# Kernel optimization log

Hardware: AMD Instinct MI355X
Metric: run time of the kernel (lower is better)

The kernel has to match this reference:

```python
import jax, jax.numpy as jnp
import numpy as np

N_NODES = 50000
N_EDGES = 800000
IN_FEAT = 100
OUT_FEAT = 100
NUM_RELS = 200
NUM_HEADS = 3
NUM_BASES = 100
SUB_IN = 1   # in_feat // num_bases
SUB_OUT = 1  # out_feat // num_bases


def setup_inputs() -> dict:
    key = jax.random.key(0)
    ks = jax.random.split(key, 10)
    return {
        "h": jax.random.normal(ks[0], (N_NODES, IN_FEAT), jnp.float32),
        "e": jax.random.normal(ks[1], (N_EDGES, IN_FEAT), jnp.float32),
        "norm": jax.random.uniform(ks[2], (N_NODES, 1), jnp.float32),
        "weight": jax.random.normal(ks[3], (NUM_RELS, NUM_BASES * SUB_IN * SUB_OUT), jnp.float32) * 0.1,
        "attn": jax.random.normal(ks[4], (NUM_RELS, NUM_HEADS, OUT_FEAT), jnp.float32) * 0.1,
        "fc_w": jax.random.normal(ks[5], (IN_FEAT, OUT_FEAT * NUM_HEADS), jnp.float32) * 0.1,
        "loop_w": jax.random.normal(ks[6], (IN_FEAT, OUT_FEAT), jnp.float32) * 0.1,
        "rel": jax.random.randint(ks[7], (N_EDGES,), 0, NUM_RELS, jnp.int32),
        "src": jax.random.randint(ks[8], (N_EDGES,), 0, N_NODES, jnp.int32),
        "dst": jax.random.randint(ks[9], (N_EDGES,), 0, N_NODES, jnp.int32),
    }


def reference(h, e, norm, weight, attn, fc_w, loop_w, rel, src, dst):
    E = rel.shape[0]
    # --- relation-indexed block-diagonal message (torch.bmm over blocks) ---
    W_e = weight[rel].reshape(E, NUM_BASES, SUB_IN, SUB_OUT)        # per-edge block weights
    h_src = h[src].reshape(E, NUM_BASES, SUB_IN)                    # gathered src features
    msg = jnp.einsum('ebi,ebio->ebo', h_src, W_e).reshape(E, OUT_FEAT)
    # --- edge-feature attention fuse ---
    a_e = attn[rel]                                                 # (E, H, OUT)
    fc_e = (e @ fc_w).reshape(E, NUM_HEADS, OUT_FEAT)               # fc(edge)
    feat = jax.nn.leaky_relu(a_e * fc_e, 0.2).sum(axis=1)           # (E, OUT)
    msg = msg + feat
    # --- scatter-sum aggregation to dst nodes, then norm + self-loop ---
    agg = jax.ops.segment_sum(msg, dst, num_segments=N_NODES)       # (N, OUT)
    node = agg * norm
    loop_message = h @ loop_w
    return node + loop_message
```

## Files before the change

### kernel.cpp

```cpp
#include <hip/hip_runtime.h>
#include <hip/hip_bf16.h>

#define N_NODES 50000
#define N_EDGES 800000
#define IN_FEAT 100
#define OUT_FEAT 100
#define NUM_RELS 200
#define NUM_HEADS 3

#define KP 128
#define NPH 112
#define NP  336
#define MB  128
#define NT_O 7
#define WPB 12

#define WS_B       0u
#define WS_LW      86016u
#define WS_CNT     114688u
#define WS_OFFS    315392u
#define WS_CURSOR  516096u
#define WS_BSUM    716800u
#define WS_PERM    717056u
#define WS_MSG     3917056u
#define NNODES_PAD 50176

typedef __attribute__((ext_vector_type(8))) short short8;
typedef __attribute__((ext_vector_type(4))) float f32x4;

__device__ __forceinline__ unsigned short f2bf(float f) {
    unsigned u = __builtin_bit_cast(unsigned, f);
    unsigned r = u + 0x7FFFu + ((u >> 16) & 1u);
    return (unsigned short)(r >> 16);
}
__device__ __forceinline__ float bf2f(unsigned hs) {
    return __builtin_bit_cast(float, hs << 16);
}

__global__ __launch_bounds__(256) void build_B(const float* __restrict__ fc_w,
                                               unsigned short* __restrict__ Bws) {
    int idx = blockIdx.x * 256 + threadIdx.x;
    if (idx >= NP * 16) return;
    int n = idx >> 4, g = idx & 15;
    int head = n / NPH, nl = n - head * NPH;
    int kt = g >> 2, g4 = g & 3;
    unsigned p[4];
#pragma unroll
    for (int half = 0; half < 2; ++half) {
#pragma unroll
        for (int jp = 0; jp < 2; ++jp) {
            int k_lo = kt * 32 + half * 16 + g4 * 4 + jp * 2;
            int k_hi = k_lo + 1;
            float vlo = (k_lo < IN_FEAT && nl < OUT_FEAT)
                      ? fc_w[k_lo * (OUT_FEAT * NUM_HEADS) + head * OUT_FEAT + nl] : 0.f;
            float vhi = (k_hi < IN_FEAT && nl < OUT_FEAT)
                      ? fc_w[k_hi * (OUT_FEAT * NUM_HEADS) + head * OUT_FEAT + nl] : 0.f;
            p[half * 2 + jp] = (unsigned)f2bf(vlo) | ((unsigned)f2bf(vhi) << 16);
        }
    }
    unsigned off = (unsigned)(head * (NPH * KP * 2)) +
                   (((unsigned)(nl * (KP * 2) + g * 16)) ^ (((unsigned)(nl & 7)) << 4));
    *reinterpret_cast<int4*>(reinterpret_cast<char*>(Bws) + off) =
        make_int4((int)p[0], (int)p[1], (int)p[2], (int)p[3]);
}

__global__ __launch_bounds__(256) void build_LW(const float* __restrict__ loop_w,
                                                unsigned short* __restrict__ LWws) {
    int idx = blockIdx.x * 256 + threadIdx.x;
    if (idx >= NPH * 16) return;
    int nl = idx >> 4, g = idx & 15;
    int kt = g >> 2, g4 = g & 3;
    unsigned p[4];
#pragma unroll
    for (int half = 0; half < 2; ++half) {
#pragma unroll
        for (int jp = 0; jp < 2; ++jp) {
            int k_lo = kt * 32 + half * 16 + g4 * 4 + jp * 2;
            int k_hi = k_lo + 1;
            float vlo = (k_lo < IN_FEAT && nl < OUT_FEAT) ? loop_w[k_lo * OUT_FEAT + nl] : 0.f;
            float vhi = (k_hi < IN_FEAT && nl < OUT_FEAT) ? loop_w[k_hi * OUT_FEAT + nl] : 0.f;
            p[half * 2 + jp] = (unsigned)f2bf(vlo) | ((unsigned)f2bf(vhi) << 16);
        }
    }
    reinterpret_cast<int4*>(LWws)[idx] = make_int4((int)p[0], (int)p[1], (int)p[2], (int)p[3]);
}

__global__ __launch_bounds__(512, 2) void loop_gemm(const float* __restrict__ h,
                                                    const unsigned short* __restrict__ LWimg,
                                                    float* __restrict__ out) {
    const int tid = threadIdx.x;
    const int wave = tid >> 6, lane = tid & 63;
    const int lrow = lane & 15, lk = lane >> 4;
    const int rbase = blockIdx.x * MB;
    const int grow = rbase + wave * 16 + lrow;
    const bool ok = grow < N_NODES;
    const float* ap = h + (size_t)grow * IN_FEAT;

    short8 afrag[4];
#pragma unroll
    for (int kt = 0; kt < 4; ++kt) {
        int k0 = kt * 32 + lk * 4, k1 = k0 + 16;
        float4 va = (ok && k0 + 4 <= IN_FEAT) ? *reinterpret_cast<const float4*>(ap + k0)
                                              : make_float4(0.f, 0.f, 0.f, 0.f);
        float4 vb = (ok && k1 + 4 <= IN_FEAT) ? *reinterpret_cast<const float4*>(ap + k1)
                                              : make_float4(0.f, 0.f, 0.f, 0.f);
        afrag[kt][0] = (short)f2bf(va.x); afrag[kt][1] = (short)f2bf(va.y);
        afrag[kt][2] = (short)f2bf(va.z); afrag[kt][3] = (short)f2bf(va.w);
        afrag[kt][4] = (short)f2bf(vb.x); afrag[kt][5] = (short)f2bf(vb.y);
        afrag[kt][6] = (short)f2bf(vb.z); afrag[kt][7] = (short)f2bf(vb.w);
    }

#pragma unroll
    for (int nt = 0; nt < NT_O; ++nt) {
        f32x4 acc = (f32x4){0.f, 0.f, 0.f, 0.f};
#pragma unroll
        for (int kt = 0; kt < 4; ++kt) {
            short8 bfrag = *reinterpret_cast<const short8*>(
                LWimg + ((nt * 16 + lrow) * KP + kt * 32 + lk * 8));
            acc = __builtin_amdgcn_mfma_f32_16x16x32_bf16(afrag[kt], bfrag, acc, 0, 0, 0);
        }
        int o = nt * 16 + lrow;
        if (o < OUT_FEAT) {
#pragma unroll
            for (int r = 0; r < 4; ++r) {
                int crow = rbase + wave * 16 + lk * 4 + r;
                if (crow < N_NODES) out[(size_t)crow * OUT_FEAT + o] = acc[r];
            }
        }
    }
}

__global__ __launch_bounds__(512) void hist_kernel(const int* __restrict__ dst,
                                                   int* __restrict__ cnt) {
    int e = blockIdx.x * 512 + threadIdx.x;
    if (e < N_EDGES) atomicAdd(&cnt[dst[e]], 1);
}

__global__ __launch_bounds__(1024) void scan1(const int* __restrict__ cnt,
                                              int* __restrict__ offs,
                                              int* __restrict__ bsum) {
    __shared__ int s[1024];
    int i = blockIdx.x * 1024 + threadIdx.x;
    int v = (i < N_NODES) ? cnt[i] : 0;
    s[threadIdx.x] = v;
    __syncthreads();
    for (int d = 1; d < 1024; d <<= 1) {
        int t = (threadIdx.x >= d) ? s[threadIdx.x - d] : 0;
        __syncthreads();
        s[threadIdx.x] += t;
        __syncthreads();
    }
    offs[i] = s[threadIdx.x] - v;
    if (threadIdx.x == 1023) bsum[blockIdx.x] = s[1023];
}

__global__ __launch_bounds__(64) void scan2(int* __restrict__ bsum) {
    __shared__ int s[64];
    int v = (threadIdx.x < NNODES_PAD / 1024) ? bsum[threadIdx.x] : 0;
    s[threadIdx.x] = v;
    __syncthreads();
    for (int d = 1; d < 64; d <<= 1) {
        int t = (threadIdx.x >= d) ? s[threadIdx.x - d] : 0;
        __syncthreads();
        s[threadIdx.x] += t;
        __syncthreads();
    }
    bsum[threadIdx.x] = s[threadIdx.x] - v;
}

__global__ __launch_bounds__(1024) void scan3(int* __restrict__ offs,
                                              const int* __restrict__ bsum,
                                              int* __restrict__ cursor) {
    int i = blockIdx.x * 1024 + threadIdx.x;
    int v = offs[i] + bsum[blockIdx.x];
    offs[i] = v;
    cursor[i] = v;
}

__global__ __launch_bounds__(512) void scatter_kernel(const int* __restrict__ dst,
                                                      int* __restrict__ cursor,
                                                      int* __restrict__ perm) {
    int e = blockIdx.x * 512 + threadIdx.x;
    if (e < N_EDGES) {
        int p = atomicAdd(&cursor[dst[e]], 1);
        perm[p] = e;
    }
}

template<bool TOWS>
__global__ __launch_bounds__(768)
__attribute__((amdgpu_waves_per_eu(3, 3)))
void feat_kernel(
        const float* __restrict__ efeat, const int* __restrict__ rel,
        const unsigned short* __restrict__ Bimg, const float* __restrict__ attn,
        const float* __restrict__ h, const float* __restrict__ weight,
        const float* __restrict__ norm, const int* __restrict__ src,
        const int* __restrict__ dst, const int* __restrict__ perm,
        float* __restrict__ out, unsigned short* __restrict__ msgws,
        int lo, int ntiles) {

    __shared__ unsigned short Blds[NP * KP];
    __shared__ unsigned short slice[WPB][16 * NPH];

    const int tid = threadIdx.x;
    {
        const int4* sp = reinterpret_cast<const int4*>(Bimg);
        int4* dp = reinterpret_cast<int4*>(Blds);
        for (int i = tid; i < NP * KP / 8; i += 768) dp[i] = sp[i];
    }
    __syncthreads();

    const int wave = tid >> 6, lane = tid & 63;
    const int lrow = lane & 15, lk = lane >> 4;
    const int gstride = gridDim.x * WPB;
    int tile = blockIdx.x * WPB + wave;
    if (tile >= ntiles) return;

    const char* Bc = reinterpret_cast<const char*>(Blds);
    int bkt[4];
#pragma unroll
    for (int kt = 0; kt < 4; ++kt)
        bkt[kt] = lrow * (KP * 2) + ((kt * 64 + lk * 16) ^ ((lrow & 7) << 4));

    float4 pa[8];
    int rl[4], sr[4], dd[4];
    {
        int slot = lo + tile * 16;
        int pe = TOWS ? perm[slot + lrow] : (slot + lrow);
        const float* ap = efeat + (size_t)pe * IN_FEAT;
#pragma unroll
        for (int kt = 0; kt < 4; ++kt) {
            int k0 = kt * 32 + lk * 4, k1 = k0 + 16;
            pa[kt * 2]     = (k0 + 4 <= IN_FEAT) ? *reinterpret_cast<const float4*>(ap + k0)
                                                 : make_float4(0.f, 0.f, 0.f, 0.f);
            pa[kt * 2 + 1] = (k1 + 4 <= IN_FEAT) ? *reinterpret_cast<const float4*>(ap + k1)
                                                 : make_float4(0.f, 0.f, 0.f, 0.f);
        }
#pragma unroll
        for (int r = 0; r < 4; ++r) {
            int pr = TOWS ? perm[slot + lk * 4 + r] : (slot + lk * 4 + r);
            rl[r] = rel[pr]; sr[r] = src[pr]; dd[r] = dst[pr];
        }
    }

    while (true) {
        const int cur = tile;
        short8 afrag[4];
#pragma unroll
        for (int kt = 0; kt < 4; ++kt) {
            float4 va = pa[kt * 2], vb = pa[kt * 2 + 1];
            afrag[kt][0] = (short)f2bf(va.x); afrag[kt][1] = (short)f2bf(va.y);
            afrag[kt][2] = (short)f2bf(va.z); afrag[kt][3] = (short)f2bf(va.w);
            afrag[kt][4] = (short)f2bf(vb.x); afrag[kt][5] = (short)f2bf(vb.y);
            afrag[kt][6] = (short)f2bf(vb.z); afrag[kt][7] = (short)f2bf(vb.w);
        }
        float nm[4]; int aoff[4]; const float* hp[4]; const float* wp[4]; int ddc[4];
#pragma unroll
        for (int r = 0; r < 4; ++r) {
            nm[r]  = norm[dd[r]];
            aoff[r] = rl[r] * (NUM_HEADS * OUT_FEAT);
            hp[r]  = h + (size_t)sr[r] * IN_FEAT;
            wp[r]  = weight + (size_t)rl[r] * OUT_FEAT;
            ddc[r] = dd[r];
        }
        float feat[NT_O][4];
#pragma unroll
        for (int nt = 0; nt < NT_O; ++nt) {
            int o = nt * 16 + lrow;
#pragma unroll
            for (int r = 0; r < 4; ++r)
                feat[nt][r] = (o < OUT_FEAT) ? hp[r][o] * wp[r][o] : 0.f;
        }
        int next = tile + gstride;
        bool more = next < ntiles;
        {
            int pidx = more ? next : cur;
            int slot = lo + pidx * 16;
            int pe = TOWS ? perm[slot + lrow] : (slot + lrow);
            const float* ap = efeat + (size_t)pe * IN_FEAT;
#pragma unroll
            for (int kt = 0; kt < 4; ++kt) {
                int k0 = kt * 32 + lk * 4, k1 = k0 + 16;
                pa[kt * 2]     = (k0 + 4 <= IN_FEAT) ? *reinterpret_cast<const float4*>(ap + k0)
                                                     : make_float4(0.f, 0.f, 0.f, 0.f);
                pa[kt * 2 + 1] = (k1 + 4 <= IN_FEAT) ? *reinterpret_cast<const float4*>(ap + k1)
                                                     : make_float4(0.f, 0.f, 0.f, 0.f);
            }
#pragma unroll
            for (int r = 0; r < 4; ++r) {
                int pr = TOWS ? perm[slot + lk * 4 + r] : (slot + lk * 4 + r);
                rl[r] = rel[pr]; sr[r] = src[pr]; dd[r] = dst[pr];
            }
        }

#pragma unroll 1
        for (int hh = 0; hh < NUM_HEADS; ++hh) {
            const char* Bh = Bc + hh * (NPH * KP * 2);
#pragma unroll
            for (int nt = 0; nt < NT_O; ++nt) {
                f32x4 acc = (f32x4){0.f, 0.f, 0.f, 0.f};
#pragma unroll
                for (int kt = 0; kt < 4; ++kt) {
                    short8 bfrag = *reinterpret_cast<const short8*>(
                        Bh + bkt[kt] + nt * 4096);
                    acc = __builtin_amdgcn_mfma_f32_16x16x32_bf16(afrag[kt], bfrag, acc, 0, 0, 0);
                }
                int o = nt * 16 + lrow;
                if (o < OUT_FEAT) {
                    int oo = hh * OUT_FEAT + o;
#pragma unroll
                    for (int r = 0; r < 4; ++r) {
                        float v = acc[r] * attn[aoff[r] + oo];
                        feat[nt][r] += (v > 0.f) ? v : 0.2f * v;
                    }
                }
            }
        }

        if (TOWS) {
            unsigned short* sl = slice[wave];
#pragma unroll
            for (int nt = 0; nt < NT_O; ++nt) {
                int o = nt * 16 + lrow;
#pragma unroll
                for (int r = 0; r < 4; ++r)
                    sl[(lk * 4 + r) * NPH + o] = f2bf(feat[nt][r] * nm[r]);
            }
            asm volatile("s_waitcnt lgkmcnt(0)" ::: "memory");
            __builtin_amdgcn_sched_barrier(0);
            const int4* sp = reinterpret_cast<const int4*>(sl);
            int4* gp = reinterpret_cast<int4*>(msgws + (size_t)cur * (16 * NPH));
            gp[lane]       = sp[lane];
            gp[lane + 64]  = sp[lane + 64];
            gp[lane + 128] = sp[lane + 128];
            if (lane < 32) gp[lane + 192] = sp[lane + 192];
        } else {
#pragma unroll
            for (int nt = 0; nt < NT_O; ++nt) {
                int o = nt * 16 + lrow;
                if (o < OUT_FEAT) {
#pragma unroll
                    for (int r = 0; r < 4; ++r)
                        atomicAdd(&out[(size_t)ddc[r] * OUT_FEAT + o], feat[nt][r] * nm[r]);
                }
            }
        }

        if (!more) break;
        tile = next;
    }
}

__global__ __launch_bounds__(256) void agg_kernel(
        const unsigned short* __restrict__ msgws, const int* __restrict__ offs,
        const int* __restrict__ cnt, float* __restrict__ out, int lo, int hi) {
    int wv = threadIdx.x >> 6, lane = threadIdx.x & 63;
    int n = blockIdx.x * 4 + wv;
    if (n >= N_NODES) return;
    int s0 = offs[n], deg = cnt[n];
    int start = s0 > lo ? s0 : lo;
    int end = (s0 + deg) < hi ? (s0 + deg) : hi;
    if (start >= end) return;
    if (lane >= OUT_FEAT / 2) return;
    const unsigned* mp = reinterpret_cast<const unsigned*>(msgws);
    float ax = 0.f, ay = 0.f;
    int k = start;
    for (; k + 2 <= end; k += 2) {
        unsigned u0 = mp[(size_t)(k - lo) * (NPH / 2) + lane];
        unsigned u1 = mp[(size_t)(k + 1 - lo) * (NPH / 2) + lane];
        ax += bf2f(u0 & 0xffffu) + bf2f(u1 & 0xffffu);
        ay += bf2f(u0 >> 16) + bf2f(u1 >> 16);
    }
    if (k < end) {
        unsigned u0 = mp[(size_t)(k - lo) * (NPH / 2) + lane];
        ax += bf2f(u0 & 0xffffu);
        ay += bf2f(u0 >> 16);
    }
    float2* op = reinterpret_cast<float2*>(out + (size_t)n * OUT_FEAT) + lane;
    float2 curv = *op;
    curv.x += ax; curv.y += ay;
    *op = curv;
}

extern "C" void kernel_launch(void* const* d_in, const int* in_sizes, int n_in,
                              void* d_out, int out_size, void* d_ws, size_t ws_size,
                              hipStream_t stream) {
    const float* h      = (const float*)d_in[0];
    const float* efeat  = (const float*)d_in[1];
    const float* norm   = (const float*)d_in[2];
    const float* weight = (const float*)d_in[3];
    const float* attn   = (const float*)d_in[4];
    const float* fc_w   = (const float*)d_in[5];
    const float* loop_w = (const float*)d_in[6];
    const int*   rel    = (const int*)d_in[7];
    const int*   src    = (const int*)d_in[8];
    const int*   dst    = (const int*)d_in[9];
    float* out = (float*)d_out;

    char* ws = (char*)d_ws;
    unsigned short* Bimg  = (unsigned short*)(ws + WS_B);
    unsigned short* LWimg = (unsigned short*)(ws + WS_LW);
    int* cnt    = (int*)(ws + WS_CNT);
    int* offs   = (int*)(ws + WS_OFFS);
    int* cursor = (int*)(ws + WS_CURSOR);
    int* bsum   = (int*)(ws + WS_BSUM);
    int* perm   = (int*)(ws + WS_PERM);
    unsigned short* msgws = (unsigned short*)(ws + WS_MSG);

    build_B<<<(NP * 16 + 255) / 256, 256, 0, stream>>>(fc_w, Bimg);
    build_LW<<<(NPH * 16 + 255) / 256, 256, 0, stream>>>(loop_w, LWimg);
    loop_gemm<<<(N_NODES + MB - 1) / MB, 512, 0, stream>>>(h, LWimg, out);

    long long avail = (long long)ws_size - (long long)WS_MSG;
    long long rows = (avail > 0) ? avail / (NPH * 2) : 0;
    rows = (rows / MB) * MB;
    if (rows > N_EDGES) rows = N_EDGES;

    if (rows >= 100000) {
        hipMemsetAsync(cnt, 0, NNODES_PAD * sizeof(int), stream);
        hist_kernel<<<(N_EDGES + 511) / 512, 512, 0, stream>>>(dst, cnt);
        scan1<<<NNODES_PAD / 1024, 1024, 0, stream>>>(cnt, offs, bsum);
        scan2<<<1, 64, 0, stream>>>(bsum);
        scan3<<<NNODES_PAD / 1024, 1024, 0, stream>>>(offs, bsum, cursor);
        scatter_kernel<<<(N_EDGES + 511) / 512, 512, 0, stream>>>(dst, cursor, perm);

        for (long long lo = 0; lo < N_EDGES; lo += rows) {
            long long hi = lo + rows; if (hi > N_EDGES) hi = N_EDGES;
            int ntiles = (int)((hi - lo) / 16);
            int nb = (ntiles + WPB - 1) / WPB; if (nb > 256) nb = 256;
            feat_kernel<true><<<nb, 768, 0, stream>>>(
                efeat, rel, Bimg, attn, h, weight, norm, src, dst, perm,
                out, msgws, (int)lo, ntiles);
            agg_kernel<<<(N_NODES + 3) / 4, 256, 0, stream>>>(
                msgws, offs, cnt, out, (int)lo, (int)hi);
        }
    } else {
        int ntiles = N_EDGES / 16;
        int nb = (ntiles + WPB - 1) / WPB; if (nb > 256) nb = 256;
        feat_kernel<false><<<nb, 768, 0, stream>>>(
            efeat, rel, Bimg, attn, h, weight, norm, src, dst, nullptr,
            out, msgws, 0, ntiles);
    }
}
```

Measured before the change: 493.6 us.

## Read edges in natural order, scatter messages to dst-sorted slots, fuse h*W in aggregation

The feature kernel now streams edge features and rel in their original order and writes each bf16 message row directly to its dst-sorted slot through a new slotmap, replacing the perm-indexed gather of efeat. The h[src]*weight[rel] product and the norm scaling move out of the feature kernel into the aggregation kernel, which gathers them through perm. Message rows shrink to 100 bf16 values and chunking over the workspace is removed in favour of a single pass. Block size and occupancy hints also change (512 threads, 8 waves per block). The trade is scattered 8-byte stores and extra gathers in agg in exchange for coalesced efeat reads.

```diff
diff --git a/kernel.cpp b/kernel.cpp
--- a/kernel.cpp
+++ b/kernel.cpp
@@ -13,7 +13,9 @@
 #define NP  336
 #define MB  128
 #define NT_O 7
-#define WPB 12
+#define WPB 8
+#define SLP 116
+#define MSGW 100
 
 #define WS_B       0u
 #define WS_LW      86016u
@@ -21,8 +23,10 @@
 #define WS_OFFS    315392u
 #define WS_CURSOR  516096u
 #define WS_BSUM    716800u
-#define WS_PERM    717056u
-#define WS_MSG     3917056u
+#define WS_SLOT    717056u
+#define WS_PERM    3917056u
+#define WS_MSG     7117056u
+#define WS_NEEDED  167117056u
 #define NNODES_PAD 50176
 
 typedef __attribute__((ext_vector_type(8))) short short8;
@@ -179,34 +183,34 @@
 
 __global__ __launch_bounds__(512) void scatter_kernel(const int* __restrict__ dst,
                                                       int* __restrict__ cursor,
-                                                      int* __restrict__ perm) {
+                                                      int* __restrict__ perm,
+                                                      int* __restrict__ slotmap) {
     int e = blockIdx.x * 512 + threadIdx.x;
     if (e < N_EDGES) {
         int p = atomicAdd(&cursor[dst[e]], 1);
         perm[p] = e;
+        slotmap[e] = p;
     }
 }
 
 template<bool TOWS>
-__global__ __launch_bounds__(768)
-__attribute__((amdgpu_waves_per_eu(3, 3)))
-void feat_kernel(
+__global__ __launch_bounds__(512, 2) void feat_kernel(
         const float* __restrict__ efeat, const int* __restrict__ rel,
         const unsigned short* __restrict__ Bimg, const float* __restrict__ attn,
         const float* __restrict__ h, const float* __restrict__ weight,
         const float* __restrict__ norm, const int* __restrict__ src,
-        const int* __restrict__ dst, const int* __restrict__ perm,
+        const int* __restrict__ dst, const int* __restrict__ slotmap,
         float* __restrict__ out, unsigned short* __restrict__ msgws,
-        int lo, int ntiles) {
-
-    __shared__ unsigned short Blds[NP * KP];
-    __shared__ unsigned short slice[WPB][16 * NPH];
+        int ntiles) {
+
+    __shared__ __align__(16) unsigned short Blds[NP * KP];
+    __shared__ __align__(16) unsigned short slice[WPB][16 * SLP];
 
     const int tid = threadIdx.x;
     {
         const int4* sp = reinterpret_cast<const int4*>(Bimg);
         int4* dp = reinterpret_cast<int4*>(Blds);
-        for (int i = tid; i < NP * KP / 8; i += 768) dp[i] = sp[i];
+        for (int i = tid; i < NP * KP / 8; i += 512) dp[i] = sp[i];
     }
     __syncthreads();
 
@@ -223,11 +227,9 @@
         bkt[kt] = lrow * (KP * 2) + ((kt * 64 + lk * 16) ^ ((lrow & 7) << 4));
 
     float4 pa[8];
-    int rl[4], sr[4], dd[4];
+    int prl[4];
     {
-        int slot = lo + tile * 16;
-        int pe = TOWS ? perm[slot + lrow] : (slot + lrow);
-        const float* ap = efeat + (size_t)pe * IN_FEAT;
+        const float* ap = efeat + (size_t)(tile * 16 + lrow) * IN_FEAT;
 #pragma unroll
         for (int kt = 0; kt < 4; ++kt) {
             int k0 = kt * 32 + lk * 4, k1 = k0 + 16;
@@ -236,15 +238,14 @@
             pa[kt * 2 + 1] = (k1 + 4 <= IN_FEAT) ? *reinterpret_cast<const float4*>(ap + k1)
                                                  : make_float4(0.f, 0.f, 0.f, 0.f);
         }
-#pragma unroll
-        for (int r = 0; r < 4; ++r) {
-            int pr = TOWS ? perm[slot + lk * 4 + r] : (slot + lk * 4 + r);
-            rl[r] = rel[pr]; sr[r] = src[pr]; dd[r] = dst[pr];
-        }
+        const int* rp = rel + tile * 16 + lk * 4;
+#pragma unroll
+        for (int r = 0; r < 4; ++r) prl[r] = rp[r];
     }
 
     while (true) {
         const int cur = tile;
+        const int tb = cur * 16;
         short8 afrag[4];
 #pragma unroll
         for (int kt = 0; kt < 4; ++kt) {
@@ -254,30 +255,15 @@
             afrag[kt][4] = (short)f2bf(vb.x); afrag[kt][5] = (short)f2bf(vb.y);
             afrag[kt][6] = (short)f2bf(vb.z); afrag[kt][7] = (short)f2bf(vb.w);
         }
-        float nm[4]; int aoff[4]; const float* hp[4]; const float* wp[4]; int ddc[4];
-#pragma unroll
-        for (int r = 0; r < 4; ++r) {
-            nm[r]  = norm[dd[r]];
-            aoff[r] = rl[r] * (NUM_HEADS * OUT_FEAT);
-            hp[r]  = h + (size_t)sr[r] * IN_FEAT;
-            wp[r]  = weight + (size_t)rl[r] * OUT_FEAT;
-            ddc[r] = dd[r];
-        }
-        float feat[NT_O][4];
-#pragma unroll
-        for (int nt = 0; nt < NT_O; ++nt) {
-            int o = nt * 16 + lrow;
-#pragma unroll
-            for (int r = 0; r < 4; ++r)
-                feat[nt][r] = (o < OUT_FEAT) ? hp[r][o] * wp[r][o] : 0.f;
-        }
+        int aoff[4];
+#pragma unroll
+        for (int r = 0; r < 4; ++r) aoff[r] = prl[r] * (NUM_HEADS * OUT_FEAT);
+
         int next = tile + gstride;
         bool more = next < ntiles;
         {
             int pidx = more ? next : cur;
-            int slot = lo + pidx * 16;
-            int pe = TOWS ? perm[slot + lrow] : (slot + lrow);
-            const float* ap = efeat + (size_t)pe * IN_FEAT;
+            const float* ap = efeat + (size_t)(pidx * 16 + lrow) * IN_FEAT;
 #pragma unroll
             for (int kt = 0; kt < 4; ++kt) {
                 int k0 = kt * 32 + lk * 4, k1 = k0 + 16;
@@ -286,12 +272,16 @@
                 pa[kt * 2 + 1] = (k1 + 4 <= IN_FEAT) ? *reinterpret_cast<const float4*>(ap + k1)
                                                      : make_float4(0.f, 0.f, 0.f, 0.f);
             }
-#pragma unroll
-            for (int r = 0; r < 4; ++r) {
-                int pr = TOWS ? perm[slot + lk * 4 + r] : (slot + lk * 4 + r);
-                rl[r] = rel[pr]; sr[r] = src[pr]; dd[r] = dst[pr];
-            }
-        }
+            const int* rp = rel + pidx * 16 + lk * 4;
+#pragma unroll
+            for (int r = 0; r < 4; ++r) prl[r] = rp[r];
+        }
+
+        float feat[NT_O][4];
+#pragma unroll
+        for (int nt = 0; nt < NT_O; ++nt)
+#pragma unroll
+            for (int r = 0; r < 4; ++r) feat[nt][r] = 0.f;
 
 #pragma unroll 1
         for (int hh = 0; hh < NUM_HEADS; ++hh) {
@@ -322,26 +312,44 @@
 #pragma unroll
             for (int nt = 0; nt < NT_O; ++nt) {
                 int o = nt * 16 + lrow;
-#pragma unroll
-                for (int r = 0; r < 4; ++r)
-                    sl[(lk * 4 + r) * NPH + o] = f2bf(feat[nt][r] * nm[r]);
+                if (o < OUT_FEAT) {
+#pragma unroll
+                    for (int r = 0; r < 4; ++r)
+                        sl[(lk * 4 + r) * SLP + o] = f2bf(feat[nt][r]);
+                }
             }
             asm volatile("s_waitcnt lgkmcnt(0)" ::: "memory");
             __builtin_amdgcn_sched_barrier(0);
-            const int4* sp = reinterpret_cast<const int4*>(sl);
-            int4* gp = reinterpret_cast<int4*>(msgws + (size_t)cur * (16 * NPH));
-            gp[lane]       = sp[lane];
-            gp[lane + 64]  = sp[lane + 64];
-            gp[lane + 128] = sp[lane + 128];
-            if (lane < 32) gp[lane + 192] = sp[lane + 192];
+            const int row = lane >> 2, part = lane & 3;
+            const int slot = slotmap[tb + row];
+            const unsigned long long* sq =
+                reinterpret_cast<const unsigned long long*>(slice[wave]);
+            unsigned long long* mq = reinterpret_cast<unsigned long long*>(msgws);
+#pragma unroll
+            for (int j = 0; j < 7; ++j) {
+                int idx = part + 4 * j;
+                if (idx < 25)
+                    mq[(size_t)slot * 25 + idx] = sq[row * (SLP / 4) + idx];
+            }
         } else {
+            int sr_r[4], d_r[4]; float nm_r[4]; int rl_r[4];
+#pragma unroll
+            for (int r = 0; r < 4; ++r) {
+                int ei = tb + lk * 4 + r;
+                sr_r[r] = src[ei]; d_r[r] = dst[ei]; nm_r[r] = norm[d_r[r]];
+                rl_r[r] = aoff[r] / (NUM_HEADS * OUT_FEAT);
+            }
 #pragma unroll
             for (int nt = 0; nt < NT_O; ++nt) {
                 int o = nt * 16 + lrow;
                 if (o < OUT_FEAT) {
 #pragma unroll
-                    for (int r = 0; r < 4; ++r)
-                        atomicAdd(&out[(size_t)ddc[r] * OUT_FEAT + o], feat[nt][r] * nm[r]);
+                    for (int r = 0; r < 4; ++r) {
+                        float mg = h[(size_t)sr_r[r] * IN_FEAT + o] *
+                                   weight[(size_t)rl_r[r] * OUT_FEAT + o];
+                        atomicAdd(&out[(size_t)d_r[r] * OUT_FEAT + o],
+                                  (mg + feat[nt][r]) * nm_r[r]);
+                    }
                 }
             }
         }
@@ -351,34 +359,46 @@
     }
 }
 
-__global__ __launch_bounds__(256) void agg_kernel(
+__global__ __launch_bounds__(256, 2) void agg_kernel(
         const unsigned short* __restrict__ msgws, const int* __restrict__ offs,
-        const int* __restrict__ cnt, float* __restrict__ out, int lo, int hi) {
+        const int* __restrict__ cnt, const int* __restrict__ perm,
+        const int* __restrict__ src, const int* __restrict__ rel,
+        const float* __restrict__ h, const float* __restrict__ weight,
+        const float* __restrict__ norm, float* __restrict__ out) {
     int wv = threadIdx.x >> 6, lane = threadIdx.x & 63;
     int n = blockIdx.x * 4 + wv;
     if (n >= N_NODES) return;
-    int s0 = offs[n], deg = cnt[n];
-    int start = s0 > lo ? s0 : lo;
-    int end = (s0 + deg) < hi ? (s0 + deg) : hi;
-    if (start >= end) return;
-    if (lane >= OUT_FEAT / 2) return;
+    int start = offs[n], deg = cnt[n];
+    if (deg == 0 || lane >= OUT_FEAT / 2) return;
     const unsigned* mp = reinterpret_cast<const unsigned*>(msgws);
     float ax = 0.f, ay = 0.f;
-    int k = start;
+    int k = start, end = start + deg;
     for (; k + 2 <= end; k += 2) {
-        unsigned u0 = mp[(size_t)(k - lo) * (NPH / 2) + lane];
-        unsigned u1 = mp[(size_t)(k + 1 - lo) * (NPH / 2) + lane];
-        ax += bf2f(u0 & 0xffffu) + bf2f(u1 & 0xffffu);
-        ay += bf2f(u0 >> 16) + bf2f(u1 >> 16);
+        int e0 = perm[k], e1 = perm[k + 1];
+        int s0 = src[e0], s1 = src[e1];
+        int r0 = rel[e0], r1 = rel[e1];
+        unsigned u0 = mp[(size_t)k * (MSGW / 2) + lane];
+        unsigned u1 = mp[(size_t)(k + 1) * (MSGW / 2) + lane];
+        float2 h0 = *reinterpret_cast<const float2*>(h + (size_t)s0 * IN_FEAT + 2 * lane);
+        float2 w0 = *reinterpret_cast<const float2*>(weight + (size_t)r0 * OUT_FEAT + 2 * lane);
+        float2 h1 = *reinterpret_cast<const float2*>(h + (size_t)s1 * IN_FEAT + 2 * lane);
+        float2 w1 = *reinterpret_cast<const float2*>(weight + (size_t)r1 * OUT_FEAT + 2 * lane);
+        ax += h0.x * w0.x + bf2f(u0 & 0xffffu) + h1.x * w1.x + bf2f(u1 & 0xffffu);
+        ay += h0.y * w0.y + bf2f(u0 >> 16) + h1.y * w1.y + bf2f(u1 >> 16);
     }
     if (k < end) {
-        unsigned u0 = mp[(size_t)(k - lo) * (NPH / 2) + lane];
-        ax += bf2f(u0 & 0xffffu);
-        ay += bf2f(u0 >> 16);
-    }
+        int e0 = perm[k];
+        int s0 = src[e0], r0 = rel[e0];
+        unsigned u0 = mp[(size_t)k * (MSGW / 2) + lane];
+        float2 h0 = *reinterpret_cast<const float2*>(h + (size_t)s0 * IN_FEAT + 2 * lane);
+        float2 w0 = *reinterpret_cast<const float2*>(weight + (size_t)r0 * OUT_FEAT + 2 * lane);
+        ax += h0.x * w0.x + bf2f(u0 & 0xffffu);
+        ay += h0.y * w0.y + bf2f(u0 >> 16);
+    }
+    float nm = norm[n];
     float2* op = reinterpret_cast<float2*>(out + (size_t)n * OUT_FEAT) + lane;
     float2 curv = *op;
-    curv.x += ax; curv.y += ay;
+    curv.x += ax * nm; curv.y += ay * nm;
     *op = curv;
 }
 
@@ -400,45 +420,36 @@
     char* ws = (char*)d_ws;
     unsigned short* Bimg  = (unsigned short*)(ws + WS_B);
     unsigned short* LWimg = (unsigned short*)(ws + WS_LW);
-    int* cnt    = (int*)(ws + WS_CNT);
-    int* offs   = (int*)(ws + WS_OFFS);
-    int* cursor = (int*)(ws + WS_CURSOR);
-    int* bsum   = (int*)(ws + WS_BSUM);
-    int* perm   = (int*)(ws + WS_PERM);
+    int* cnt     = (int*)(ws + WS_CNT);
+    int* offs    = (int*)(ws + WS_OFFS);
+    int* cursor  = (int*)(ws + WS_CURSOR);
+    int* bsum    = (int*)(ws + WS_BSUM);
+    int* slotmap = (int*)(ws + WS_SLOT);
+    int* perm    = (int*)(ws + WS_PERM);
     unsigned short* msgws = (unsigned short*)(ws + WS_MSG);
 
     build_B<<<(NP * 16 + 255) / 256, 256, 0, stream>>>(fc_w, Bimg);
     build_LW<<<(NPH * 16 + 255) / 256, 256, 0, stream>>>(loop_w, LWimg);
     loop_gemm<<<(N_NODES + MB - 1) / MB, 512, 0, stream>>>(h, LWimg, out);
 
-    long long avail = (long long)ws_size - (long long)WS_MSG;
-    long long rows = (avail > 0) ? avail / (NPH * 2) : 0;
-    rows = (rows / MB) * MB;
-    if (rows > N_EDGES) rows = N_EDGES;
-
-    if (rows >= 100000) {
+    const int ntiles = N_EDGES / 16;
+
+    if (ws_size >= (size_t)WS_NEEDED) {
         hipMemsetAsync(cnt, 0, NNODES_PAD * sizeof(int), stream);
         hist_kernel<<<(N_EDGES + 511) / 512, 512, 0, stream>>>(dst, cnt);
         scan1<<<NNODES_PAD / 1024, 1024, 0, stream>>>(cnt, offs, bsum);
         scan2<<<1, 64, 0, stream>>>(bsum);
         scan3<<<NNODES_PAD / 1024, 1024, 0, stream>>>(offs, bsum, cursor);
-        scatter_kernel<<<(N_EDGES + 511) / 512, 512, 0, stream>>>(dst, cursor, perm);
-
-        for (long long lo = 0; lo < N_EDGES; lo += rows) {
-            long long hi = lo + rows; if (hi > N_EDGES) hi = N_EDGES;
-            int ntiles = (int)((hi - lo) / 16);
-            int nb = (ntiles + WPB - 1) / WPB; if (nb > 256) nb = 256;
-            feat_kernel<true><<<nb, 768, 0, stream>>>(
-                efeat, rel, Bimg, attn, h, weight, norm, src, dst, perm,
-                out, msgws, (int)lo, ntiles);
-            agg_kernel<<<(N_NODES + 3) / 4, 256, 0, stream>>>(
-                msgws, offs, cnt, out, (int)lo, (int)hi);
-        }
+        scatter_kernel<<<(N_EDGES + 511) / 512, 512, 0, stream>>>(dst, cursor, perm, slotmap);
+
+        feat_kernel<true><<<256, 512, 0, stream>>>(
+            efeat, rel, Bimg, attn, h, weight, norm, src, dst, slotmap,
+            out, msgws, ntiles);
+        agg_kernel<<<(N_NODES + 3) / 4, 256, 0, stream>>>(
+            msgws, offs, cnt, perm, src, rel, h, weight, norm, out);
     } else {
-        int ntiles = N_EDGES / 16;
-        int nb = (ntiles + WPB - 1) / WPB; if (nb > 256) nb = 256;
-        feat_kernel<false><<<nb, 768, 0, stream>>>(
+        feat_kernel<false><<<256, 512, 0, stream>>>(
             efeat, rel, Bimg, attn, h, weight, norm, src, dst, nullptr,
-            out, msgws, 0, ntiles);
-    }
-}
+            out, msgws, ntiles);
+    }
+}
```

After: 440.2 us. -10.8%, faster.
